# Kernel tuning notes

Hardware: AMD Instinct MI355X
Metric: run time of the kernel (lower is better)

Reference implementation:

```python
import jax, jax.numpy as jnp
import numpy as np
from jax import lax

B, C, H, W = 4, 64, 64, 64
CH = C // 2  # edge_detect hidden channels
BN_EPS = 1e-5


def conv1x1(x, w, b):
    # x: (B,C,H,W), w: (O,C), b: (O,)
    return jnp.einsum('bchw,oc->bohw', x, w) + b[None, :, None, None]


def setup_inputs() -> dict:
    key = jax.random.key(0)
    ks = jax.random.split(key, 12)
    s = 1.0 / np.sqrt(C)
    inp = {
        'x': jax.random.normal(ks[0], (B, C, H, W), jnp.float32),
        'Wq': jax.random.normal(ks[1], (C, C), jnp.float32) * s,
        'bq': jnp.zeros((C,), jnp.float32),
        'Wk': jax.random.normal(ks[2], (C, C), jnp.float32) * s,
        'bk': jnp.zeros((C,), jnp.float32),
        'Wv': jax.random.normal(ks[3], (C, C), jnp.float32) * s,
        'bv': jnp.zeros((C,), jnp.float32),
        'We1': jax.random.normal(ks[4], (CH, C, 3, 3), jnp.float32) * (1.0 / np.sqrt(C * 9)),
        'be1': jnp.zeros((CH,), jnp.float32),
        'bn_w': jnp.ones((CH,), jnp.float32),
        'bn_b': jnp.zeros((CH,), jnp.float32),
        'bn_mean': jnp.zeros((CH,), jnp.float32),
        'bn_var': jnp.ones((CH,), jnp.float32),
        'We2': jax.random.normal(ks[5], (1, CH), jnp.float32) * (1.0 / np.sqrt(CH)),
        'be2': jnp.zeros((1,), jnp.float32),
        'gamma': jax.random.normal(ks[6], (1,), jnp.float32) * 0.1,
        'beta': jax.random.normal(ks[7], (1,), jnp.float32) * 0.1,
    }
    return inp


def reference(x, Wq, bq, Wk, bk, Wv, bv, We1, be1, bn_w, bn_b, bn_mean, bn_var, We2, be2, gamma, beta):
    b, c, h, w = x.shape
    hw = h * w
    q = conv1x1(x, Wq, bq).reshape(b, c, hw).transpose(0, 2, 1)  # (B,HW,C)
    k = conv1x1(x, Wk, bk).reshape(b, c, hw)                      # (B,C,HW)
    v = conv1x1(x, Wv, bv).reshape(b, c, hw)                      # (B,C,HW)

    energy = jnp.einsum('bnc,bcm->bnm', q, k)                      # (B,HW,HW)
    attention = jax.nn.softmax(energy, axis=-1)

    # edge_detect: 3x3 conv -> BN (eval stats) -> ReLU -> 1x1 conv -> sigmoid
    e = lax.conv_general_dilated(x, We1, (1, 1), 'SAME',
                                 dimension_numbers=('NCHW', 'OIHW', 'NCHW'))
    e = e + be1[None, :, None, None]
    e = (e - bn_mean[None, :, None, None]) * jax.lax.rsqrt(bn_var + BN_EPS)[None, :, None, None]
    e = e * bn_w[None, :, None, None] + bn_b[None, :, None, None]
    e = jax.nn.relu(e)
    e = conv1x1(e, We2, be2)                                       # (B,1,H,W)
    edge = jax.nn.sigmoid(e).reshape(b, 1, hw)                     # (B,1,HW)

    fa = attention * (1.0 + beta[0] * edge)                        # broadcast over query dim
    denom = jnp.maximum(jnp.sum(jnp.abs(fa), axis=2, keepdims=True), 1e-12)
    fa = fa / denom                                                # L1 renorm along keys

    out = jnp.einsum('bcm,bnm->bcn', v, fa).reshape(b, c, h, w)
    return gamma[0] * out + x
```

## Files before the change

### kernel.cpp

```cpp
#include <hip/hip_runtime.h>
#include <hip/hip_bf16.h>

typedef unsigned short u16;
typedef __attribute__((ext_vector_type(8))) __bf16 bf16x8;
typedef __attribute__((ext_vector_type(4))) float f32x4;
typedef __attribute__((ext_vector_type(16))) float f32x16;


#define NSPLIT 8

__device__ __forceinline__ u16 f2bf(float f) {
    unsigned u = __builtin_bit_cast(unsigned, f);
    u += 0x7FFFu + ((u >> 16) & 1u);
    return (u16)(u >> 16);
}
__device__ __forceinline__ float bf2f(u16 v) {
    unsigned u = ((unsigned)v) << 16;
    return __builtin_bit_cast(float, u);
}

__global__ __launch_bounds__(256) void qkv_edge_kernel(
    const float* __restrict__ x,
    const float* __restrict__ Wq, const float* __restrict__ bq,
    const float* __restrict__ Wk, const float* __restrict__ bk,
    const float* __restrict__ Wv, const float* __restrict__ bv,
    const float* __restrict__ We1, const float* __restrict__ be1,
    const float* __restrict__ bn_w, const float* __restrict__ bn_b,
    const float* __restrict__ bn_mean, const float* __restrict__ bn_var,
    const float* __restrict__ We2, const float* __restrict__ be2,
    const float* __restrict__ beta,
    u16* __restrict__ Qt, u16* __restrict__ Kt, u16* __restrict__ Vm)
{
    __shared__ __align__(16) u16 sm[33280];
    const int t = threadIdx.x;
    const int wv = t >> 6, lane = t & 63;
    const int quad = lane >> 4, l15 = lane & 15;

    if (blockIdx.x < 256) {
        u16* Wl   = sm;
        u16* xt_s = sm + 13824;
        u16* vt   = sm + 13824 + 4224;
        const int b = blockIdx.x >> 6;
        const int n0 = (blockIdx.x & 63) << 6;

        const float* Wmat[3] = {Wq, Wk, Wv};
#pragma unroll
        for (int m = 0; m < 3; ++m)
#pragma unroll
            for (int i = 0; i < 4; ++i) {
                int u = t + i * 256;
                float4 w4 = *reinterpret_cast<const float4*>(Wmat[m] + u * 4);
                int row = u >> 4, col = (u & 15) * 4;
                uint2 pk;
                pk.x = (unsigned)f2bf(w4.x) | ((unsigned)f2bf(w4.y) << 16);
                pk.y = (unsigned)f2bf(w4.z) | ((unsigned)f2bf(w4.w) << 16);
                *reinterpret_cast<uint2*>(&Wl[(m * 64 + row) * 72 + col]) = pk;
            }
        for (int i = 0; i < 16; ++i) {
            int lin = t + i * 256;
            int c = lin >> 6, nn = lin & 63;
            xt_s[nn * 66 + c] = f2bf(x[(size_t)(b * 64 + c) * 4096 + n0 + nn]);
        }
        __syncthreads();

        bf16x8 bx[2];
#pragma unroll
        for (int h = 0; h < 2; ++h)
            bx[h] = *reinterpret_cast<const bf16x8*>(
                &xt_s[(wv * 16 + l15) * 66 + h * 32 + quad * 8]);

        f32x4 d[3][4];
#pragma unroll
        for (int m = 0; m < 3; ++m)
#pragma unroll
            for (int mt = 0; mt < 4; ++mt) d[m][mt] = (f32x4){0.f, 0.f, 0.f, 0.f};

#pragma unroll
        for (int h = 0; h < 2; ++h)
#pragma unroll
            for (int m = 0; m < 3; ++m)
#pragma unroll
                for (int mt = 0; mt < 4; ++mt) {
                    bf16x8 af = *reinterpret_cast<const bf16x8*>(
                        &Wl[(m * 64 + mt * 16 + l15) * 72 + h * 32 + quad * 8]);
                    d[m][mt] = __builtin_amdgcn_mfma_f32_16x16x32_bf16(af, bx[h], d[m][mt], 0, 0, 0);
                }

        const float* bias[3] = {bq, bk, bv};
        const float L2E = 1.44269504f;
#pragma unroll
        for (int m = 0; m < 3; ++m)
#pragma unroll
            for (int mt = 0; mt < 4; ++mt) {
                float4 bi = *reinterpret_cast<const float4*>(bias[m] + mt * 16 + quad * 4);
                d[m][mt][0] += bi.x; d[m][mt][1] += bi.y; d[m][mt][2] += bi.z; d[m][mt][3] += bi.w;
                if (m == 0) {
                    d[m][mt][0] *= L2E; d[m][mt][1] *= L2E;
                    d[m][mt][2] *= L2E; d[m][mt][3] *= L2E;
                }
            }

        const int rowchunk = (n0 >> 4) + wv;
        {
            u16* baseQ = Qt + (size_t)b * 262144;
#pragma unroll
            for (int mt = 0; mt < 4; ++mt) {
                uint2 pk;
                pk.x = (unsigned)f2bf(d[0][mt][0]) | ((unsigned)f2bf(d[0][mt][1]) << 16);
                pk.y = (unsigned)f2bf(d[0][mt][2]) | ((unsigned)f2bf(d[0][mt][3]) << 16);
                *reinterpret_cast<uint2*>(
                    baseQ + ((size_t)(rowchunk * 8 + mt * 2 + (quad >> 1))) * 128 +
                    l15 * 8 + (quad & 1) * 4) = pk;
            }
        }
        {
            u16* baseK = Kt + (size_t)b * 327680 + (size_t)(n0 >> 6) * 5120;
#pragma unroll
            for (int mt = 0; mt < 4; ++mt) {
                uint2 pk;
                pk.x = (unsigned)f2bf(d[1][mt][0]) | ((unsigned)f2bf(d[1][mt][1]) << 16);
                pk.y = (unsigned)f2bf(d[1][mt][2]) | ((unsigned)f2bf(d[1][mt][3]) << 16);
                *reinterpret_cast<uint2*>(
                    baseK + (size_t)(wv * 8 + mt * 2 + (quad >> 1)) * 128 +
                    l15 * 8 + (quad & 1) * 4) = pk;
            }
        }
#pragma unroll
        for (int mt = 0; mt < 4; ++mt)
#pragma unroll
            for (int r = 0; r < 4; ++r)
                vt[(mt * 16 + quad * 4 + r) * 72 + wv * 16 + l15] = f2bf(d[2][mt][r]);
        __syncthreads();
        {
            u16* Vb_st = Vm + (size_t)b * 262144;
            const int kt = n0 >> 6;
#pragma unroll
            for (int i = 0; i < 2; ++i) {
                int unit = t + i * 256;
                int f = unit >> 7, hq = (unit >> 4) & 7, cl = unit & 15;
                const u16* src = &vt[(f * 16 + cl) * 72 + hq * 8];
                uint4 v4 = *reinterpret_cast<const uint4*>(src);
                *reinterpret_cast<uint4*>(
                    Vb_st + ((size_t)((kt * 4 + f) * 8 + hq)) * 128 + cl * 8) = v4;
            }
        }
    } else {
        u16* Ae_s = sm;
        u16* xr_s = sm + 18688;
        const int eb = blockIdx.x - 256;
        const int b = eb >> 6, h = eb & 63;

        if (t < 192) {
            int kh = t / 64, rem = t & 63;
            int col = (rem >> 5) * 65, ci2 = (rem & 31) * 2;
            *reinterpret_cast<unsigned*>(&xr_s[(kh * 66 + col) * 72 + ci2]) = 0u;
        }
#pragma unroll
        for (int i = 0; i < 18; ++i) {
            int u = t + i * 256;
            int ch = u / 144;
            int rem = u - ch * 144;
            int p = rem >> 4, cig = (rem & 15) * 4;
            const float* src = We1 + ch * 576 + cig * 9 + p;
            float a = src[0], b2 = src[9], c2 = src[18], d2 = src[27];
            uint2 pk;
            pk.x = (unsigned)f2bf(a) | ((unsigned)f2bf(b2) << 16);
            pk.y = (unsigned)f2bf(c2) | ((unsigned)f2bf(d2) << 16);
            *reinterpret_cast<uint2*>(&Ae_s[ch * 584 + p * 64 + cig]) = pk;
        }
#pragma unroll
        for (int i = 0; i < 12; ++i) {
            int u = t + i * 256;
            int w = u & 63, cig = (u >> 6) & 15, kh = u >> 10;
            int hs = h + kh - 1;
            float v0 = 0.f, v1 = 0.f, v2 = 0.f, v3 = 0.f;
            if ((unsigned)hs < 64u) {
                const float* src = x + ((size_t)(b * 64 + cig * 4) * 64 + hs) * 64 + w;
                v0 = src[0]; v1 = src[4096]; v2 = src[8192]; v3 = src[12288];
            }
            uint2 pk;
            pk.x = (unsigned)f2bf(v0) | ((unsigned)f2bf(v1) << 16);
            pk.y = (unsigned)f2bf(v2) | ((unsigned)f2bf(v3) << 16);
            *reinterpret_cast<uint2*>(&xr_s[(kh * 66 + w + 1) * 72 + cig * 4]) = pk;
        }
        __syncthreads();

        f32x4 e[2];
        e[0] = (f32x4){0.f, 0.f, 0.f, 0.f};
        e[1] = (f32x4){0.f, 0.f, 0.f, 0.f};
#pragma unroll
        for (int p = 0; p < 9; ++p) {
            const int kh = p / 3, kw = p - kh * 3;
#pragma unroll
            for (int half = 0; half < 2; ++half) {
                bf16x8 bfr = *reinterpret_cast<const bf16x8*>(
                    &xr_s[(kh * 66 + wv * 16 + l15 + kw) * 72 + half * 32 + quad * 8]);
#pragma unroll
                for (int mt = 0; mt < 2; ++mt) {
                    bf16x8 af = *reinterpret_cast<const bf16x8*>(
                        &Ae_s[(mt * 16 + l15) * 584 + p * 64 + half * 32 + quad * 8]);
                    e[mt] = __builtin_amdgcn_mfma_f32_16x16x32_bf16(af, bfr, e[mt], 0, 0, 0);
                }
            }
        }
        float partial = 0.f;
#pragma unroll
        for (int mt = 0; mt < 2; ++mt) {
            float4 bw = *reinterpret_cast<const float4*>(bn_w    + mt * 16 + quad * 4);
            float4 bb = *reinterpret_cast<const float4*>(bn_b    + mt * 16 + quad * 4);
            float4 bm = *reinterpret_cast<const float4*>(bn_mean + mt * 16 + quad * 4);
            float4 bv2 = *reinterpret_cast<const float4*>(bn_var + mt * 16 + quad * 4);
            float4 b1 = *reinterpret_cast<const float4*>(be1     + mt * 16 + quad * 4);
            float4 w2 = *reinterpret_cast<const float4*>(We2     + mt * 16 + quad * 4);
            float sc, sh;
            sc = bw.x * rsqrtf(bv2.x + 1e-5f); sh = (b1.x - bm.x) * sc + bb.x;
            partial += fmaxf(e[mt][0] * sc + sh, 0.f) * w2.x;
            sc = bw.y * rsqrtf(bv2.y + 1e-5f); sh = (b1.y - bm.y) * sc + bb.y;
            partial += fmaxf(e[mt][1] * sc + sh, 0.f) * w2.y;
            sc = bw.z * rsqrtf(bv2.z + 1e-5f); sh = (b1.z - bm.z) * sc + bb.z;
            partial += fmaxf(e[mt][2] * sc + sh, 0.f) * w2.z;
            sc = bw.w * rsqrtf(bv2.w + 1e-5f); sh = (b1.w - bm.w) * sc + bb.w;
            partial += fmaxf(e[mt][3] * sc + sh, 0.f) * w2.w;
        }
        partial += __shfl_xor(partial, 16);
        partial += __shfl_xor(partial, 32);
        if (lane < 16) {
            float s = partial + be2[0];
            float sg = 1.f / (1.f + __expf(-s));
            float lwp = __log2f(fmaxf(1.f + beta[0] * sg, 1e-20f));
            u16* k5 = Kt + (size_t)b * 327680 + (size_t)h * 5120 + 4096 +
                      (wv >> 1) * 512 + (wv & 1) * 256 + lane * 8;
            uint4 st0;
            st0.x = (unsigned)f2bf(lwp) | 0x3F800000u;
            st0.y = 0u; st0.z = 0u; st0.w = 0u;
            *reinterpret_cast<uint4*>(k5) = st0;
            uint4 z; z.x = 0u; z.y = 0u; z.z = 0u; z.w = 0u;
            *reinterpret_cast<uint4*>(k5 + 128) = z;
        }
    }
}

__global__ __launch_bounds__(256, 2) void attn_kernel(
    const u16* __restrict__ Qt, const u16* __restrict__ Kt,
    const u16* __restrict__ Vm,
    u16* __restrict__ O_part, float* __restrict__ l_part)
{
    constexpr int KT_ITERS = 64 / NSPLIT;
    const int bid = ((blockIdx.x & 7) << 7) + (blockIdx.x >> 3);
    const int t = threadIdx.x;
    const int qi = bid / NSPLIT;
    const int split = bid % NSPLIT;
    const int b = qi >> 5;
    const int n0 = (qi & 31) << 7;
    const int wv = t >> 6, lane = t & 63;
    const int l31 = lane & 31, hi = lane >> 5;
    const int i4 = (lane >> 4) & 1, l15 = lane & 15;

    const int kvoff = i4 * 1024 + hi * 128 + l15 * 8;
    const int k5off = i4 * 256 + hi * 128 + l15 * 8;
    const u16* Qb  = Qt + (size_t)b * 262144;
    const u16* Ksp = Kt + (size_t)b * 327680 + (size_t)(split * KT_ITERS) * 5120;
    const u16* Vsp = Vm + (size_t)b * 262144 + (size_t)(split * KT_ITERS) * 4096;

    bf16x8 qf[4];
#pragma unroll
    for (int kc = 0; kc < 4; ++kc)
        qf[kc] = __builtin_bit_cast(bf16x8, *reinterpret_cast<const uint4*>(
            Qb + (size_t)(((n0 >> 4) + wv * 2) * 1024) + kvoff + kc * 256));
    uint4 qc5u;
    qc5u.x = hi ? 0u : 0xC18A3F80u;
    qc5u.y = 0u; qc5u.z = 0u; qc5u.w = 0u;
    const bf16x8 qc5 = __builtin_bit_cast(bf16x8, qc5u);

    uint4 kf[2][5];
    uint4 vf[2][4];
#pragma unroll
    for (int tl = 0; tl < 2; ++tl) {
#pragma unroll
        for (int kc = 0; kc < 4; ++kc)
            kf[tl][kc] = *reinterpret_cast<const uint4*>(Ksp + tl * 2048 + kc * 256 + kvoff);
        kf[tl][4] = *reinterpret_cast<const uint4*>(Ksp + 4096 + tl * 512 + k5off);
    }
#pragma unroll
    for (int ct = 0; ct < 2; ++ct)
#pragma unroll
        for (int kc = 0; kc < 4; ++kc)
            vf[ct][kc] = *reinterpret_cast<const uint4*>(Vsp + ct * 2048 + kc * 256 + kvoff);

    f32x16 o[2];
#pragma unroll
    for (int ct = 0; ct < 2; ++ct)
#pragma unroll
        for (int i = 0; i < 16; ++i) o[ct][i] = 0.f;
    float lacc = 0.f;

    for (int kt = 0; kt < KT_ITERS; ++kt) {
        f32x16 s0, s1;
#pragma unroll
        for (int i = 0; i < 16; ++i) { s0[i] = 0.f; s1[i] = 0.f; }
        __builtin_amdgcn_s_setprio(1);
        s0 = __builtin_amdgcn_mfma_f32_32x32x16_bf16(__builtin_bit_cast(bf16x8, kf[0][4]), qc5,   s0, 0, 0, 0);
        s0 = __builtin_amdgcn_mfma_f32_32x32x16_bf16(__builtin_bit_cast(bf16x8, kf[0][0]), qf[0], s0, 0, 0, 0);
        s0 = __builtin_amdgcn_mfma_f32_32x32x16_bf16(__builtin_bit_cast(bf16x8, kf[0][1]), qf[1], s0, 0, 0, 0);
        s0 = __builtin_amdgcn_mfma_f32_32x32x16_bf16(__builtin_bit_cast(bf16x8, kf[0][2]), qf[2], s0, 0, 0, 0);
        s0 = __builtin_amdgcn_mfma_f32_32x32x16_bf16(__builtin_bit_cast(bf16x8, kf[0][3]), qf[3], s0, 0, 0, 0);
        s1 = __builtin_amdgcn_mfma_f32_32x32x16_bf16(__builtin_bit_cast(bf16x8, kf[1][4]), qc5,   s1, 0, 0, 0);
        s1 = __builtin_amdgcn_mfma_f32_32x32x16_bf16(__builtin_bit_cast(bf16x8, kf[1][0]), qf[0], s1, 0, 0, 0);
        s1 = __builtin_amdgcn_mfma_f32_32x32x16_bf16(__builtin_bit_cast(bf16x8, kf[1][1]), qf[1], s1, 0, 0, 0);
        s1 = __builtin_amdgcn_mfma_f32_32x32x16_bf16(__builtin_bit_cast(bf16x8, kf[1][2]), qf[2], s1, 0, 0, 0);
        s1 = __builtin_amdgcn_mfma_f32_32x32x16_bf16(__builtin_bit_cast(bf16x8, kf[1][3]), qf[3], s1, 0, 0, 0);
        __builtin_amdgcn_s_setprio(0);

        const int ktn = (kt + 1) & (KT_ITERS - 1);
        {
            const u16* Kn = Ksp + (size_t)ktn * 5120;
#pragma unroll
            for (int tl = 0; tl < 2; ++tl) {
#pragma unroll
                for (int kc = 0; kc < 4; ++kc)
                    kf[tl][kc] = *reinterpret_cast<const uint4*>(Kn + tl * 2048 + kc * 256 + kvoff);
                kf[tl][4] = *reinterpret_cast<const uint4*>(Kn + 4096 + tl * 512 + k5off);
            }
        }

        uint4 pbu[2][2];
#pragma unroll
        for (int tl = 0; tl < 2; ++tl) {
            const f32x16& sv = tl ? s1 : s0;
            float p[16];
#pragma unroll
            for (int i = 0; i < 16; ++i) p[i] = exp2f(sv[i]);
            float t0 = (p[0] + p[1]) + (p[2] + p[3]);
            float t1 = (p[4] + p[5]) + (p[6] + p[7]);
            float t2 = (p[8] + p[9]) + (p[10] + p[11]);
            float t3 = (p[12] + p[13]) + (p[14] + p[15]);
            lacc += (t0 + t1) + (t2 + t3);
#pragma unroll
            for (int kc2 = 0; kc2 < 2; ++kc2) {
                int a0, a1, b0, b1;
                asm("v_cvt_pk_bf16_f32 %0, %1, %2" : "=v"(a0) : "v"(p[kc2 * 8 + 0]), "v"(p[kc2 * 8 + 1]));
                asm("v_cvt_pk_bf16_f32 %0, %1, %2" : "=v"(a1) : "v"(p[kc2 * 8 + 2]), "v"(p[kc2 * 8 + 3]));
                asm("v_cvt_pk_bf16_f32 %0, %1, %2" : "=v"(b0) : "v"(p[kc2 * 8 + 4]), "v"(p[kc2 * 8 + 5]));
                asm("v_cvt_pk_bf16_f32 %0, %1, %2" : "=v"(b1) : "v"(p[kc2 * 8 + 6]), "v"(p[kc2 * 8 + 7]));
                auto swA = __builtin_amdgcn_permlane32_swap(a0, b0, false, false);
                auto swB = __builtin_amdgcn_permlane32_swap(a1, b1, false, false);
                uint4 fr;
                fr.x = (unsigned)swA[0];
                fr.y = (unsigned)swB[0];
                fr.z = (unsigned)swA[1];
                fr.w = (unsigned)swB[1];
                pbu[tl][kc2] = fr;
            }
        }

        __builtin_amdgcn_s_setprio(1);
#pragma unroll
        for (int ct = 0; ct < 2; ++ct) {
            o[ct] = __builtin_amdgcn_mfma_f32_32x32x16_bf16(__builtin_bit_cast(bf16x8, vf[ct][0]),
                        __builtin_bit_cast(bf16x8, pbu[0][0]), o[ct], 0, 0, 0);
            o[ct] = __builtin_amdgcn_mfma_f32_32x32x16_bf16(__builtin_bit_cast(bf16x8, vf[ct][1]),
                        __builtin_bit_cast(bf16x8, pbu[0][1]), o[ct], 0, 0, 0);
            o[ct] = __builtin_amdgcn_mfma_f32_32x32x16_bf16(__builtin_bit_cast(bf16x8, vf[ct][2]),
                        __builtin_bit_cast(bf16x8, pbu[1][0]), o[ct], 0, 0, 0);
            o[ct] = __builtin_amdgcn_mfma_f32_32x32x16_bf16(__builtin_bit_cast(bf16x8, vf[ct][3]),
                        __builtin_bit_cast(bf16x8, pbu[1][1]), o[ct], 0, 0, 0);
        }
        __builtin_amdgcn_s_setprio(0);

        {
            const u16* Vn = Vsp + (size_t)ktn * 4096;
#pragma unroll
            for (int ct = 0; ct < 2; ++ct)
#pragma unroll
                for (int kc = 0; kc < 4; ++kc)
                    vf[ct][kc] = *reinterpret_cast<const uint4*>(Vn + ct * 2048 + kc * 256 + kvoff);
        }
    }

    float ltot = lacc + __shfl_xor(lacc, 32);
    if (lane < 32)
        l_part[(size_t)bid * 128 + wv * 32 + lane] = ltot;

    const size_t pbase = (size_t)bid * 8192;
    const int q = wv * 32 + l31;
#pragma unroll
    for (int ct = 0; ct < 2; ++ct)
#pragma unroll
        for (int g = 0; g < 4; ++g) {
            int w0, w1;
            asm("v_cvt_pk_bf16_f32 %0, %1, %2" : "=v"(w0) : "v"(o[ct][4 * g + 0]), "v"(o[ct][4 * g + 1]));
            asm("v_cvt_pk_bf16_f32 %0, %1, %2" : "=v"(w1) : "v"(o[ct][4 * g + 2]), "v"(o[ct][4 * g + 3]));
            uint2 pk2;
            pk2.x = (unsigned)w0;
            pk2.y = (unsigned)w1;
            *reinterpret_cast<uint2*>(
                &O_part[pbase + (size_t)(ct * 8 + g * 2 + hi) * 512 + q * 4]) = pk2;
        }
}

__global__ __launch_bounds__(256) void combine_kernel(
    const u16* __restrict__ O_part, const float* __restrict__ l_part,
    const float* __restrict__ x, const float* __restrict__ g_gamma,
    float* __restrict__ out)
{
    __shared__ float ot[32 * 65];
    __shared__ float ls[32];
    const int t = threadIdx.x;
    const int ab = blockIdx.x >> 2;
    const int sub = blockIdx.x & 3;
    const int b = ab >> 5;
    const int n0 = (ab & 31) << 7;
    const float gamma = g_gamma[0];

#pragma unroll
    for (int i = 0; i < 2; ++i) {
        int idx = t + i * 256;
        int c4 = idx >> 5, ql = idx & 31;
        float a0 = 0.f, a1 = 0.f, a2 = 0.f, a3 = 0.f;
#pragma unroll
        for (int s4 = 0; s4 < NSPLIT; ++s4) {
            uint2 u = *reinterpret_cast<const uint2*>(
                O_part + ((size_t)(ab * NSPLIT + s4)) * 8192 +
                (size_t)c4 * 512 + (sub * 32 + ql) * 4);
            a0 += bf2f((u16)(u.x & 0xFFFF));
            a1 += bf2f((u16)(u.x >> 16));
            a2 += bf2f((u16)(u.y & 0xFFFF));
            a3 += bf2f((u16)(u.y >> 16));
        }
        ot[ql * 65 + c4 * 4 + 0] = a0;
        ot[ql * 65 + c4 * 4 + 1] = a1;
        ot[ql * 65 + c4 * 4 + 2] = a2;
        ot[ql * 65 + c4 * 4 + 3] = a3;
    }
    if (t < 32) {
        float lsum = 0.f;
#pragma unroll
        for (int s4 = 0; s4 < NSPLIT; ++s4)
            lsum += l_part[((size_t)(ab * NSPLIT + s4)) * 128 + sub * 32 + t];
        ls[t] = gamma / fmaxf(lsum, 1e-30f);
    }
    __syncthreads();
    {
        const int c = t >> 2, seg = t & 3;
        const size_t gbase = ((size_t)(b * 64 + c)) * 4096 + n0 + sub * 32 + seg * 8;
#pragma unroll
        for (int j = 0; j < 2; ++j) {
            float4 xv = *reinterpret_cast<const float4*>(&x[gbase + j * 4]);
            float4 rv;
            int nl = seg * 8 + j * 4;
            rv.x = ot[(nl + 0) * 65 + c] * ls[nl + 0] + xv.x;
            rv.y = ot[(nl + 1) * 65 + c] * ls[nl + 1] + xv.y;
            rv.z = ot[(nl + 2) * 65 + c] * ls[nl + 2] + xv.z;
            rv.w = ot[(nl + 3) * 65 + c] * ls[nl + 3] + xv.w;
            *reinterpret_cast<float4*>(&out[gbase + j * 4]) = rv;
        }
    }
}

extern "C" void kernel_launch(void* const* d_in, const int* in_sizes, int n_in,
                              void* d_out, int out_size, void* d_ws, size_t ws_size,
                              hipStream_t stream) {
    const float* x      = (const float*)d_in[0];
    const float* Wq     = (const float*)d_in[1];
    const float* bq     = (const float*)d_in[2];
    const float* Wk     = (const float*)d_in[3];
    const float* bk     = (const float*)d_in[4];
    const float* Wv     = (const float*)d_in[5];
    const float* bv     = (const float*)d_in[6];
    const float* We1    = (const float*)d_in[7];
    const float* be1    = (const float*)d_in[8];
    const float* bn_w   = (const float*)d_in[9];
    const float* bn_b   = (const float*)d_in[10];
    const float* bn_mean= (const float*)d_in[11];
    const float* bn_var = (const float*)d_in[12];
    const float* We2    = (const float*)d_in[13];
    const float* be2    = (const float*)d_in[14];
    const float* gamma  = (const float*)d_in[15];
    const float* beta   = (const float*)d_in[16];

    char* ws = (char*)d_ws;
    const size_t MB = 1024 * 1024;
    u16*   Qt     = (u16*)ws;
    u16*   Kt     = (u16*)(ws + 2 * MB);
    u16*   Vm     = (u16*)(ws + 5 * MB);
    float* l_part = (float*)(ws + 7 * MB);
    u16*   O_part = (u16*)(ws + 8 * MB);

    float* out = (float*)d_out;

    qkv_edge_kernel<<<dim3(512), dim3(256), 0, stream>>>(
        x, Wq, bq, Wk, bk, Wv, bv, We1, be1, bn_w, bn_b, bn_mean, bn_var,
        We2, be2, beta, Qt, Kt, Vm);
    attn_kernel<<<dim3(128 * NSPLIT), dim3(256), 0, stream>>>(
        Qt, Kt, Vm, O_part, l_part);
    combine_kernel<<<dim3(512), dim3(256), 0, stream>>>(
        O_part, l_part, x, gamma, out);
}
```

Before: 136.0 us.

## Stage K/V tiles through double-buffered LDS via global_load_lds in attention kernel

Replaces per-wave register prefetch of K and V tiles, where each of the four waves loaded the full tile from global memory, with cooperative global-to-LDS direct loads into a double buffer. Each tile is now fetched once per block and shared across waves, which cuts redundant global/L2 traffic and frees VGPRs, and launch bounds are raised to 3 blocks per SM. In exchange it adds a block barrier every iteration and LDS read latency before the MFMAs. The async LDS loads rely on the barrier for ordering, which may not wait on vmcnt for direct-to-LDS loads.

```diff
diff --git a/kernel.cpp b/kernel.cpp
--- a/kernel.cpp
+++ b/kernel.cpp
@@ -17,6 +17,11 @@
 __device__ __forceinline__ float bf2f(u16 v) {
     unsigned u = ((unsigned)v) << 16;
     return __builtin_bit_cast(float, u);
+}
+__device__ __forceinline__ void gl_lds16(const u16* g, u16* l) {
+    __builtin_amdgcn_global_load_lds(
+        (const __attribute__((address_space(1))) unsigned*)g,
+        (__attribute__((address_space(3))) unsigned*)l, 16, 0, 0);
 }
 
 __global__ __launch_bounds__(256) void qkv_edge_kernel(
@@ -240,12 +245,14 @@
     }
 }
 
-__global__ __launch_bounds__(256, 2) void attn_kernel(
+__global__ __launch_bounds__(256, 3) void attn_kernel(
     const u16* __restrict__ Qt, const u16* __restrict__ Kt,
     const u16* __restrict__ Vm,
     u16* __restrict__ O_part, float* __restrict__ l_part)
 {
     constexpr int KT_ITERS = 64 / NSPLIT;
+    __shared__ __align__(16) u16 kv[2][9216];
+
     const int bid = ((blockIdx.x & 7) << 7) + (blockIdx.x >> 3);
     const int t = threadIdx.x;
     const int qi = bid / NSPLIT;
@@ -272,20 +279,21 @@
     qc5u.y = 0u; qc5u.z = 0u; qc5u.w = 0u;
     const bf16x8 qc5 = __builtin_bit_cast(bf16x8, qc5u);
 
-    uint4 kf[2][5];
-    uint4 vf[2][4];
-#pragma unroll
-    for (int tl = 0; tl < 2; ++tl) {
-#pragma unroll
-        for (int kc = 0; kc < 4; ++kc)
-            kf[tl][kc] = *reinterpret_cast<const uint4*>(Ksp + tl * 2048 + kc * 256 + kvoff);
-        kf[tl][4] = *reinterpret_cast<const uint4*>(Ksp + 4096 + tl * 512 + k5off);
-    }
-#pragma unroll
-    for (int ct = 0; ct < 2; ++ct)
-#pragma unroll
-        for (int kc = 0; kc < 4; ++kc)
-            vf[ct][kc] = *reinterpret_cast<const uint4*>(Vsp + ct * 2048 + kc * 256 + kvoff);
+    auto STAGE = [&](int buf, int tile) {
+        if (wv < 2) {
+            const u16* Kg = Ksp + (size_t)tile * 5120 + (wv * 320 + lane) * 8;
+            u16* Kl = &kv[buf][(wv * 320 + lane) * 8];
+#pragma unroll
+            for (int i = 0; i < 5; ++i)
+                gl_lds16(Kg + i * 512, Kl + i * 512);
+        } else {
+            const u16* Vg = Vsp + (size_t)tile * 4096 + ((wv - 2) * 256 + lane) * 8;
+            u16* Vl = &kv[buf][5120 + ((wv - 2) * 256 + lane) * 8];
+#pragma unroll
+            for (int i = 0; i < 4; ++i)
+                gl_lds16(Vg + i * 512, Vl + i * 512);
+        }
+    };
 
     f32x16 o[2];
 #pragma unroll
@@ -294,42 +302,38 @@
         for (int i = 0; i < 16; ++i) o[ct][i] = 0.f;
     float lacc = 0.f;
 
+    STAGE(0, 0);
+    __syncthreads();
+
+    int cur = 0;
     for (int kt = 0; kt < KT_ITERS; ++kt) {
-        f32x16 s0, s1;
-#pragma unroll
-        for (int i = 0; i < 16; ++i) { s0[i] = 0.f; s1[i] = 0.f; }
-        __builtin_amdgcn_s_setprio(1);
-        s0 = __builtin_amdgcn_mfma_f32_32x32x16_bf16(__builtin_bit_cast(bf16x8, kf[0][4]), qc5,   s0, 0, 0, 0);
-        s0 = __builtin_amdgcn_mfma_f32_32x32x16_bf16(__builtin_bit_cast(bf16x8, kf[0][0]), qf[0], s0, 0, 0, 0);
-        s0 = __builtin_amdgcn_mfma_f32_32x32x16_bf16(__builtin_bit_cast(bf16x8, kf[0][1]), qf[1], s0, 0, 0, 0);
-        s0 = __builtin_amdgcn_mfma_f32_32x32x16_bf16(__builtin_bit_cast(bf16x8, kf[0][2]), qf[2], s0, 0, 0, 0);
-        s0 = __builtin_amdgcn_mfma_f32_32x32x16_bf16(__builtin_bit_cast(bf16x8, kf[0][3]), qf[3], s0, 0, 0, 0);
-        s1 = __builtin_amdgcn_mfma_f32_32x32x16_bf16(__builtin_bit_cast(bf16x8, kf[1][4]), qc5,   s1, 0, 0, 0);
-        s1 = __builtin_amdgcn_mfma_f32_32x32x16_bf16(__builtin_bit_cast(bf16x8, kf[1][0]), qf[0], s1, 0, 0, 0);
-        s1 = __builtin_amdgcn_mfma_f32_32x32x16_bf16(__builtin_bit_cast(bf16x8, kf[1][1]), qf[1], s1, 0, 0, 0);
-        s1 = __builtin_amdgcn_mfma_f32_32x32x16_bf16(__builtin_bit_cast(bf16x8, kf[1][2]), qf[2], s1, 0, 0, 0);
-        s1 = __builtin_amdgcn_mfma_f32_32x32x16_bf16(__builtin_bit_cast(bf16x8, kf[1][3]), qf[3], s1, 0, 0, 0);
-        __builtin_amdgcn_s_setprio(0);
-
-        const int ktn = (kt + 1) & (KT_ITERS - 1);
-        {
-            const u16* Kn = Ksp + (size_t)ktn * 5120;
-#pragma unroll
-            for (int tl = 0; tl < 2; ++tl) {
-#pragma unroll
-                for (int kc = 0; kc < 4; ++kc)
-                    kf[tl][kc] = *reinterpret_cast<const uint4*>(Kn + tl * 2048 + kc * 256 + kvoff);
-                kf[tl][4] = *reinterpret_cast<const uint4*>(Kn + 4096 + tl * 512 + k5off);
-            }
-        }
+        if (kt + 1 < KT_ITERS) STAGE(cur ^ 1, kt + 1);
+
+        const u16* Kl = &kv[cur][0];
+        const u16* Vl = &kv[cur][5120];
 
         uint4 pbu[2][2];
 #pragma unroll
         for (int tl = 0; tl < 2; ++tl) {
-            const f32x16& sv = tl ? s1 : s0;
+            bf16x8 k4 = *reinterpret_cast<const bf16x8*>(Kl + 4096 + tl * 512 + k5off);
+            bf16x8 k0 = *reinterpret_cast<const bf16x8*>(Kl + tl * 2048 + kvoff);
+            bf16x8 k1 = *reinterpret_cast<const bf16x8*>(Kl + tl * 2048 + 256 + kvoff);
+            bf16x8 k2 = *reinterpret_cast<const bf16x8*>(Kl + tl * 2048 + 512 + kvoff);
+            bf16x8 k3 = *reinterpret_cast<const bf16x8*>(Kl + tl * 2048 + 768 + kvoff);
+            f32x16 s;
+#pragma unroll
+            for (int i = 0; i < 16; ++i) s[i] = 0.f;
+            __builtin_amdgcn_s_setprio(1);
+            s = __builtin_amdgcn_mfma_f32_32x32x16_bf16(k4, qc5,   s, 0, 0, 0);
+            s = __builtin_amdgcn_mfma_f32_32x32x16_bf16(k0, qf[0], s, 0, 0, 0);
+            s = __builtin_amdgcn_mfma_f32_32x32x16_bf16(k1, qf[1], s, 0, 0, 0);
+            s = __builtin_amdgcn_mfma_f32_32x32x16_bf16(k2, qf[2], s, 0, 0, 0);
+            s = __builtin_amdgcn_mfma_f32_32x32x16_bf16(k3, qf[3], s, 0, 0, 0);
+            __builtin_amdgcn_s_setprio(0);
+
             float p[16];
 #pragma unroll
-            for (int i = 0; i < 16; ++i) p[i] = exp2f(sv[i]);
+            for (int i = 0; i < 16; ++i) p[i] = exp2f(s[i]);
             float t0 = (p[0] + p[1]) + (p[2] + p[3]);
             float t1 = (p[4] + p[5]) + (p[6] + p[7]);
             float t2 = (p[8] + p[9]) + (p[10] + p[11]);
@@ -353,28 +357,26 @@
             }
         }
 
-        __builtin_amdgcn_s_setprio(1);
 #pragma unroll
         for (int ct = 0; ct < 2; ++ct) {
-            o[ct] = __builtin_amdgcn_mfma_f32_32x32x16_bf16(__builtin_bit_cast(bf16x8, vf[ct][0]),
+            bf16x8 v0 = *reinterpret_cast<const bf16x8*>(Vl + ct * 2048 + kvoff);
+            bf16x8 v1 = *reinterpret_cast<const bf16x8*>(Vl + ct * 2048 + 256 + kvoff);
+            bf16x8 v2 = *reinterpret_cast<const bf16x8*>(Vl + ct * 2048 + 512 + kvoff);
+            bf16x8 v3 = *reinterpret_cast<const bf16x8*>(Vl + ct * 2048 + 768 + kvoff);
+            __builtin_amdgcn_s_setprio(1);
+            o[ct] = __builtin_amdgcn_mfma_f32_32x32x16_bf16(v0,
                         __builtin_bit_cast(bf16x8, pbu[0][0]), o[ct], 0, 0, 0);
-            o[ct] = __builtin_amdgcn_mfma_f32_32x32x16_bf16(__builtin_bit_cast(bf16x8, vf[ct][1]),
+            o[ct] = __builtin_amdgcn_mfma_f32_32x32x16_bf16(v1,
                         __builtin_bit_cast(bf16x8, pbu[0][1]), o[ct], 0, 0, 0);
-            o[ct] = __builtin_amdgcn_mfma_f32_32x32x16_bf16(__builtin_bit_cast(bf16x8, vf[ct][2]),
+            o[ct] = __builtin_amdgcn_mfma_f32_32x32x16_bf16(v2,
                         __builtin_bit_cast(bf16x8, pbu[1][0]), o[ct], 0, 0, 0);
-            o[ct] = __builtin_amdgcn_mfma_f32_32x32x16_bf16(__builtin_bit_cast(bf16x8, vf[ct][3]),
+            o[ct] = __builtin_amdgcn_mfma_f32_32x32x16_bf16(v3,
                         __builtin_bit_cast(bf16x8, pbu[1][1]), o[ct], 0, 0, 0);
-        }
-        __builtin_amdgcn_s_setprio(0);
-
-        {
-            const u16* Vn = Vsp + (size_t)ktn * 4096;
-#pragma unroll
-            for (int ct = 0; ct < 2; ++ct)
-#pragma unroll
-                for (int kc = 0; kc < 4; ++kc)
-                    vf[ct][kc] = *reinterpret_cast<const uint4*>(Vn + ct * 2048 + kc * 256 + kvoff);
-        }
+            __builtin_amdgcn_s_setprio(0);
+        }
+
+        __syncthreads();
+        cur ^= 1;
     }
 
     float ltot = lacc + __shfl_xor(lacc, 32);
```

After: 174.2 us. 28.1% more time.
